# Performance work log

Measured on AMD Instinct MI355X. Metric: run time of the kernel, lower is better.

The kernel has to match this reference:

```python
import jax, jax.numpy as jnp
import numpy as np

C = 3               # BSARec cutoff hyperparameter
CUTOFF = max(1, C // 2 + 1)  # number of low-frequency bins kept = 2
LN_EPS = 1e-5       # torch LayerNorm default


def setup_inputs() -> dict:
    key = jax.random.key(0)
    k1, k2 = jax.random.split(key)
    B, S, H = 64, 2048, 256
    x = jax.random.normal(k1, (B, S, H), dtype=jnp.float32)
    sqrt_beta = jax.random.normal(k2, (1, 1, H), dtype=jnp.float32)
    ln_weight = jnp.ones((H,), dtype=jnp.float32)
    ln_bias = jnp.zeros((H,), dtype=jnp.float32)
    return {"x": x, "sqrt_beta": sqrt_beta, "ln_weight": ln_weight, "ln_bias": ln_bias}


def _layer_norm(h, weight, bias):
    mean = jnp.mean(h, axis=-1, keepdims=True)
    var = jnp.mean(jnp.square(h - mean), axis=-1, keepdims=True)
    return (h - mean) * jax.lax.rsqrt(var + LN_EPS) * weight + bias


def reference(x, sqrt_beta, ln_weight, ln_bias):
    B, S, H = x.shape
    # orthonormal rFFT along the sequence axis
    x_fft = jnp.fft.rfft(x, axis=1, norm="ortho")          # [B, S//2+1, H] complex
    freq_bins = x_fft.shape[1]
    cutoff = min(freq_bins, CUTOFF)
    # zero all bins >= cutoff (low-pass)
    bin_idx = jnp.arange(freq_bins)[None, :, None]
    low_fft = jnp.where(bin_idx < cutoff, x_fft, 0.0 + 0.0j)
    low_pass = jnp.fft.irfft(low_fft, n=S, axis=1, norm="ortho")  # [B, S, H]
    high_pass = x - low_pass
    seq = low_pass + jnp.square(sqrt_beta) * high_pass
    # dropout is identity at eval time
    return _layer_norm(seq + x, ln_weight, ln_bias)
```

## Files before the change

kernel.cpp:

```cpp
#include <hip/hip_runtime.h>

#define B_DIM 64
#define S_LEN 2048
#define H_DIM 256
#define TWO_PI 6.283185307179586f

typedef float f32x4 __attribute__((ext_vector_type(4)));

__global__ __launch_bounds__(256) void k_partial(const float* __restrict__ x,
                                                 float* __restrict__ partials,
                                                 int rows_per_split, int nsplit_b) {
    const int b = blockIdx.x;
    const int split = blockIdx.y;
    const int tid = threadIdx.x;
    const int lane = tid & 63;
    const int wave = tid >> 6;
    const int h0 = lane * 4;

    const int rows_per_wave = rows_per_split >> 2;
    const int t0 = split * rows_per_split + wave * rows_per_wave;
    const float* px = x + ((size_t)b * S_LEN + t0) * H_DIM + h0;
    const float wfreq = TWO_PI / (float)S_LEN;

    f32x4 s0v = {0.f, 0.f, 0.f, 0.f};
    f32x4 c1v = {0.f, 0.f, 0.f, 0.f};
    f32x4 s1v = {0.f, 0.f, 0.f, 0.f};

    for (int r = 0; r < rows_per_wave; r += 2) {
        const f32x4 v0 = *reinterpret_cast<const f32x4*>(px + (size_t)r * H_DIM);
        const f32x4 v1 = *reinterpret_cast<const f32x4*>(px + (size_t)(r + 1) * H_DIM);
        float sn0, cs0, sn1, cs1;
        __sincosf(wfreq * (float)(t0 + r), &sn0, &cs0);
        __sincosf(wfreq * (float)(t0 + r + 1), &sn1, &cs1);
        s0v += v0 + v1;
        c1v += v0 * cs0 + v1 * cs1;
        s1v += v0 * sn0 + v1 * sn1;
    }

    __shared__ float red[4][3 * H_DIM];
#pragma unroll
    for (int j = 0; j < 4; ++j) {
        red[wave][0 * H_DIM + h0 + j] = s0v[j];
        red[wave][1 * H_DIM + h0 + j] = c1v[j];
        red[wave][2 * H_DIM + h0 + j] = s1v[j];
    }
    __syncthreads();

#pragma unroll
    for (int k = 0; k < 3; ++k) {
        const int v = tid + k * 256;
        const float acc = red[0][v] + red[1][v] + red[2][v] + red[3][v];
        partials[((size_t)(split * B_DIM + b)) * (3 * H_DIM) + v] = acc;
    }
}

__global__ __launch_bounds__(256) void k_reduce(const float* __restrict__ partials,
                                                float* __restrict__ sums,
                                                int nsplit) {
    const int j = blockIdx.x * 256 + threadIdx.x;
    float acc = 0.f;
    for (int s = 0; s < nsplit; ++s)
        acc += partials[(size_t)s * (B_DIM * 3 * H_DIM) + j];
    sums[j] = acc;
}

#define FROWS 32
__global__ __launch_bounds__(256) void k_final(const float* __restrict__ x,
                                               const float* __restrict__ sums,
                                               const float* __restrict__ sqrt_beta,
                                               const float* __restrict__ lnw,
                                               const float* __restrict__ lnb,
                                               float* __restrict__ out) {
    const int blocks_per_b = S_LEN / FROWS;
    const int b = blockIdx.x / blocks_per_b;
    const int tchunk = blockIdx.x % blocks_per_b;
    const int tid = threadIdx.x;
    const int lane = tid & 63;
    const int wave = tid >> 6;
    const int h0 = lane * 4;

    const f32x4 S0 = *reinterpret_cast<const f32x4*>(sums + b * 768 + h0);
    const f32x4 C1 = *reinterpret_cast<const f32x4*>(sums + b * 768 + 256 + h0);
    const f32x4 S1 = *reinterpret_cast<const f32x4*>(sums + b * 768 + 512 + h0);
    const f32x4 sb = *reinterpret_cast<const f32x4*>(sqrt_beta + h0);
    const f32x4 Wv = *reinterpret_cast<const f32x4*>(lnw + h0);
    const f32x4 Bv = *reinterpret_cast<const f32x4*>(lnb + h0);
    const f32x4 b2 = sb * sb;
    const f32x4 CA = b2 + 1.f;
    const f32x4 CB = 1.f - b2;

    const float invS = 1.f / (float)S_LEN;
    const float wfreq = TWO_PI / (float)S_LEN;
    const int tbase = tchunk * FROWS + wave * (FROWS / 4);
    const float* __restrict__ pxr = x + ((size_t)b * S_LEN + tbase) * H_DIM + h0;
    float* __restrict__ por = out + ((size_t)b * S_LEN + tbase) * H_DIM + h0;

#pragma unroll
    for (int r = 0; r < FROWS / 4; ++r) {
        float sn, cs;
        __sincosf(wfreq * (float)(tbase + r), &sn, &cs);

        const f32x4 v = *reinterpret_cast<const f32x4*>(pxr + (size_t)r * H_DIM);
        const f32x4 lp = (S0 + (C1 * cs + S1 * sn) * 2.f) * invS;
        const f32x4 y = CB * lp + CA * v;

        float sum = y.x + y.y + y.z + y.w;
        float sumsq = y.x * y.x + y.y * y.y + y.z * y.z + y.w * y.w;
#pragma unroll
        for (int m = 1; m < 64; m <<= 1) {
            sum += __shfl_xor(sum, m, 64);
            sumsq += __shfl_xor(sumsq, m, 64);
        }
        const float mean = sum * (1.f / (float)H_DIM);
        const float var = sumsq * (1.f / (float)H_DIM) - mean * mean;
        const float rstd = rsqrtf(var + 1e-5f);

        f32x4 o = (y - mean) * rstd * Wv + Bv;
        __builtin_nontemporal_store(o, reinterpret_cast<f32x4*>(por + (size_t)r * H_DIM));
    }
}

extern "C" void kernel_launch(void* const* d_in, const int* in_sizes, int n_in,
                              void* d_out, int out_size, void* d_ws, size_t ws_size,
                              hipStream_t stream) {
    const float* x  = (const float*)d_in[0];
    const float* sb = (const float*)d_in[1];
    const float* w  = (const float*)d_in[2];
    const float* bi = (const float*)d_in[3];
    float* out = (float*)d_out;

    int nsplit = 32;
    while (nsplit > 1 &&
           ((size_t)(nsplit + 1) * B_DIM * 3 * H_DIM * sizeof(float)) > ws_size)
        nsplit >>= 1;
    float* partials = (float*)d_ws;
    float* sums = partials + (size_t)nsplit * B_DIM * 3 * H_DIM;

    k_partial<<<dim3(B_DIM, nsplit), 256, 0, stream>>>(x, partials, S_LEN / nsplit, nsplit);
    k_reduce<<<(B_DIM * 3 * H_DIM) / 256, 256, 0, stream>>>(partials, sums, nsplit);
    k_final<<<B_DIM * (S_LEN / FROWS), 256, 0, stream>>>(x, sums, sb, w, bi, out);
}
```

Before: 81.98 us.

## Fuse partial, reduce and final kernels into one cooperative grid-synced kernel

Replaces the three-kernel pipeline with a single cooperative kernel of one 1024-thread block per CU, which computes the low-frequency partial sums, writes them to workspace, grid-syncs, then applies the low-pass and LayerNorm to the same rows. This removes two launches and the separate reduce pass, and makes each block re-read its own slice of x soon after the first pass so it may hit in cache. It relies on all 256 blocks being co-resident and trades occupancy and a grid-wide barrier for these savings.

```diff
diff --git a/kernel.cpp b/kernel.cpp
--- a/kernel.cpp
+++ b/kernel.cpp
@@ -1,43 +1,52 @@
 #include <hip/hip_runtime.h>
+#include <hip/hip_cooperative_groups.h>
+
+namespace cg = cooperative_groups;
 
 #define B_DIM 64
 #define S_LEN 2048
 #define H_DIM 256
 #define TWO_PI 6.283185307179586f
+#define NBLK 256
+#define NTHR 1024
+#define WAVES 16
+#define ROWS_PER_BLK 512
 
 typedef float f32x4 __attribute__((ext_vector_type(4)));
 
-__global__ __launch_bounds__(256) void k_partial(const float* __restrict__ x,
-                                                 float* __restrict__ partials,
-                                                 int rows_per_split, int nsplit_b) {
-    const int b = blockIdx.x;
-    const int split = blockIdx.y;
+__global__ __launch_bounds__(NTHR) void k_fused(const float* __restrict__ x,
+                                                const float* __restrict__ sqrt_beta,
+                                                const float* __restrict__ lnw,
+                                                const float* __restrict__ lnb,
+                                                float* __restrict__ out,
+                                                float* __restrict__ ws) {
+    const int blk = blockIdx.x;
+    const int b = blk >> 2;
+    const int q = blk & 3;
     const int tid = threadIdx.x;
     const int lane = tid & 63;
     const int wave = tid >> 6;
     const int h0 = lane * 4;
 
-    const int rows_per_wave = rows_per_split >> 2;
-    const int t0 = split * rows_per_split + wave * rows_per_wave;
-    const float* px = x + ((size_t)b * S_LEN + t0) * H_DIM + h0;
     const float wfreq = TWO_PI / (float)S_LEN;
+    const int t_base = q * ROWS_PER_BLK;
+    const float* __restrict__ px = x + ((size_t)b * S_LEN + t_base) * H_DIM + h0;
 
     f32x4 s0v = {0.f, 0.f, 0.f, 0.f};
     f32x4 c1v = {0.f, 0.f, 0.f, 0.f};
     f32x4 s1v = {0.f, 0.f, 0.f, 0.f};
-
-    for (int r = 0; r < rows_per_wave; r += 2) {
+    for (int r = wave; r < ROWS_PER_BLK; r += 2 * WAVES) {
         const f32x4 v0 = *reinterpret_cast<const f32x4*>(px + (size_t)r * H_DIM);
-        const f32x4 v1 = *reinterpret_cast<const f32x4*>(px + (size_t)(r + 1) * H_DIM);
+        const f32x4 v1 = *reinterpret_cast<const f32x4*>(px + (size_t)(r + WAVES) * H_DIM);
         float sn0, cs0, sn1, cs1;
-        __sincosf(wfreq * (float)(t0 + r), &sn0, &cs0);
-        __sincosf(wfreq * (float)(t0 + r + 1), &sn1, &cs1);
+        __sincosf(wfreq * (float)(t_base + r), &sn0, &cs0);
+        __sincosf(wfreq * (float)(t_base + r + WAVES), &sn1, &cs1);
         s0v += v0 + v1;
         c1v += v0 * cs0 + v1 * cs1;
         s1v += v0 * sn0 + v1 * sn1;
     }
 
-    __shared__ float red[4][3 * H_DIM];
+    __shared__ float red[WAVES][3 * H_DIM];
 #pragma unroll
     for (int j = 0; j < 4; ++j) {
         red[wave][0 * H_DIM + h0 + j] = s0v[j];
@@ -45,62 +54,39 @@
         red[wave][2 * H_DIM + h0 + j] = s1v[j];
     }
     __syncthreads();
+    if (tid < 3 * H_DIM) {
+        float acc = 0.f;
+#pragma unroll
+        for (int w = 0; w < WAVES; ++w) acc += red[w][tid];
+        ws[(size_t)blk * (3 * H_DIM) + tid] = acc;
+    }
 
+    cg::this_grid().sync();
+
+    f32x4 S0 = {0.f, 0.f, 0.f, 0.f};
+    f32x4 C1 = {0.f, 0.f, 0.f, 0.f};
+    f32x4 S1 = {0.f, 0.f, 0.f, 0.f};
 #pragma unroll
-    for (int k = 0; k < 3; ++k) {
-        const int v = tid + k * 256;
-        const float acc = red[0][v] + red[1][v] + red[2][v] + red[3][v];
-        partials[((size_t)(split * B_DIM + b)) * (3 * H_DIM) + v] = acc;
+    for (int k = 0; k < 4; ++k) {
+        const float* p = ws + (size_t)((blk & ~3) + k) * (3 * H_DIM);
+        S0 += *reinterpret_cast<const f32x4*>(p + h0);
+        C1 += *reinterpret_cast<const f32x4*>(p + H_DIM + h0);
+        S1 += *reinterpret_cast<const f32x4*>(p + 2 * H_DIM + h0);
     }
-}
 
-__global__ __launch_bounds__(256) void k_reduce(const float* __restrict__ partials,
-                                                float* __restrict__ sums,
-                                                int nsplit) {
-    const int j = blockIdx.x * 256 + threadIdx.x;
-    float acc = 0.f;
-    for (int s = 0; s < nsplit; ++s)
-        acc += partials[(size_t)s * (B_DIM * 3 * H_DIM) + j];
-    sums[j] = acc;
-}
-
-#define FROWS 32
-__global__ __launch_bounds__(256) void k_final(const float* __restrict__ x,
-                                               const float* __restrict__ sums,
-                                               const float* __restrict__ sqrt_beta,
-                                               const float* __restrict__ lnw,
-                                               const float* __restrict__ lnb,
-                                               float* __restrict__ out) {
-    const int blocks_per_b = S_LEN / FROWS;
-    const int b = blockIdx.x / blocks_per_b;
-    const int tchunk = blockIdx.x % blocks_per_b;
-    const int tid = threadIdx.x;
-    const int lane = tid & 63;
-    const int wave = tid >> 6;
-    const int h0 = lane * 4;
-
-    const f32x4 S0 = *reinterpret_cast<const f32x4*>(sums + b * 768 + h0);
-    const f32x4 C1 = *reinterpret_cast<const f32x4*>(sums + b * 768 + 256 + h0);
-    const f32x4 S1 = *reinterpret_cast<const f32x4*>(sums + b * 768 + 512 + h0);
     const f32x4 sb = *reinterpret_cast<const f32x4*>(sqrt_beta + h0);
     const f32x4 Wv = *reinterpret_cast<const f32x4*>(lnw + h0);
     const f32x4 Bv = *reinterpret_cast<const f32x4*>(lnb + h0);
     const f32x4 b2 = sb * sb;
     const f32x4 CA = b2 + 1.f;
     const f32x4 CB = 1.f - b2;
+    const float invS = 1.f / (float)S_LEN;
 
-    const float invS = 1.f / (float)S_LEN;
-    const float wfreq = TWO_PI / (float)S_LEN;
-    const int tbase = tchunk * FROWS + wave * (FROWS / 4);
-    const float* __restrict__ pxr = x + ((size_t)b * S_LEN + tbase) * H_DIM + h0;
-    float* __restrict__ por = out + ((size_t)b * S_LEN + tbase) * H_DIM + h0;
-
-#pragma unroll
-    for (int r = 0; r < FROWS / 4; ++r) {
+    float* __restrict__ po = out + ((size_t)b * S_LEN + t_base) * H_DIM + h0;
+    for (int r = wave; r < ROWS_PER_BLK; r += WAVES) {
         float sn, cs;
-        __sincosf(wfreq * (float)(tbase + r), &sn, &cs);
-
-        const f32x4 v = *reinterpret_cast<const f32x4*>(pxr + (size_t)r * H_DIM);
+        __sincosf(wfreq * (float)(t_base + r), &sn, &cs);
+        const f32x4 v = *reinterpret_cast<const f32x4*>(px + (size_t)r * H_DIM);
         const f32x4 lp = (S0 + (C1 * cs + S1 * sn) * 2.f) * invS;
         const f32x4 y = CB * lp + CA * v;
 
@@ -116,7 +102,7 @@
         const float rstd = rsqrtf(var + 1e-5f);
 
         f32x4 o = (y - mean) * rstd * Wv + Bv;
-        __builtin_nontemporal_store(o, reinterpret_cast<f32x4*>(por + (size_t)r * H_DIM));
+        __builtin_nontemporal_store(o, reinterpret_cast<f32x4*>(po + (size_t)r * H_DIM));
     }
 }
 
@@ -128,15 +114,10 @@
     const float* w  = (const float*)d_in[2];
     const float* bi = (const float*)d_in[3];
     float* out = (float*)d_out;
+    float* ws = (float*)d_ws;
 
-    int nsplit = 32;
-    while (nsplit > 1 &&
-           ((size_t)(nsplit + 1) * B_DIM * 3 * H_DIM * sizeof(float)) > ws_size)
-        nsplit >>= 1;
-    float* partials = (float*)d_ws;
-    float* sums = partials + (size_t)nsplit * B_DIM * 3 * H_DIM;
-
-    k_partial<<<dim3(B_DIM, nsplit), 256, 0, stream>>>(x, partials, S_LEN / nsplit, nsplit);
-    k_reduce<<<(B_DIM * 3 * H_DIM) / 256, 256, 0, stream>>>(partials, sums, nsplit);
-    k_final<<<B_DIM * (S_LEN / FROWS), 256, 0, stream>>>(x, sums, sb, w, bi, out);
+    void* args[] = {(void*)&x, (void*)&sb, (void*)&w, (void*)&bi,
+                    (void*)&out, (void*)&ws};
+    hipLaunchCooperativeKernel((const void*)k_fused, dim3(NBLK), dim3(NTHR),
+                               args, 0, stream);
 }
```

New measurement: 102.0 us. 1.24x slower.
